# Performance work log

Measured on AMD Instinct MI355X. Metric: run time of the kernel, lower is better.

## Reference

```python
import jax, jax.numpy as jnp
import numpy as np

ITEM_NUM = 50000
TARGET_ITEM_NUM = 50000
EMB = 128
N_LAYERS = 3
N_EDGES = 800000
N_NODES = ITEM_NUM + 1  # forward uses item_emb[:item_num+1]


def gcn_conv(x, row, col, W, b, n):
    """PyG GCNConv: symmetric-normalized aggregation with self-loops.
    out = D^{-1/2} (A + I) D^{-1/2} (x @ W) + b
    """
    h = x @ W  # [n, d]
    loops = jnp.arange(n)
    r = jnp.concatenate([row, loops])  # source
    c = jnp.concatenate([col, loops])  # target
    deg = jax.ops.segment_sum(jnp.ones(r.shape[0], x.dtype), c, num_segments=n)
    dinv = jnp.where(deg > 0, deg ** -0.5, jnp.zeros_like(deg))
    norm = dinv[r] * dinv[c]  # [E+n]
    out = jax.ops.segment_sum(h[r] * norm[:, None], c, num_segments=n)
    return out + b


def setup_inputs() -> dict:
    key = jax.random.key(0)
    k0, k1, k2 = jax.random.split(key, 3)
    edge_index = jax.random.randint(k0, (2, N_EDGES), 0, N_NODES)
    total = ITEM_NUM + TARGET_ITEM_NUM + 1
    # xavier_uniform for embedding table and per-layer GCN weights
    lim_e = float(np.sqrt(6.0 / (total + EMB)))
    item_emb = jax.random.uniform(k1, (total, EMB), jnp.float32, -lim_e, lim_e)
    lim_w = float(np.sqrt(6.0 / (EMB + EMB)))
    W = jax.random.uniform(k2, (N_LAYERS, EMB, EMB), jnp.float32, -lim_w, lim_w)
    b = jnp.zeros((N_LAYERS, EMB), jnp.float32)
    return {"edge_index": edge_index, "item_emb": item_emb, "W": W, "b": b}


def reference(edge_index, item_emb, W, b):
    n = N_NODES
    row, col = edge_index[0], edge_index[1]
    embeds = [item_emb[:n]]
    for i in range(N_LAYERS):
        embeds.append(gcn_conv(embeds[-1], row, col, W[i], b[i], n))
    return sum(embeds)  # [n, EMB], sum over layer embeddings
```

## Files before the change

### kernel.cpp

```cpp
#include <hip/hip_runtime.h>
#include <hip/hip_bf16.h>


constexpr int NN   = 50001;
constexpr int D    = 128;
constexpr int NPAD = 50048;
constexpr int NBK  = 196;
constexpr int CAP  = 7680;
constexpr int ZROW = NPAD - 1;

using bf16x8 = __attribute__((ext_vector_type(8))) short;
using f32x4  = __attribute__((ext_vector_type(4))) float;
using u16x8  = __attribute__((ext_vector_type(8))) unsigned short;
using u32x4  = __attribute__((ext_vector_type(4))) unsigned;

__device__ __forceinline__ ushort f2b(float f) {
    unsigned u = __float_as_uint(f);
    return (ushort)((u + 0x7FFFu + ((u >> 16) & 1u)) >> 16);
}
__device__ __forceinline__ float b2f(ushort u) {
    return __uint_as_float((unsigned)u << 16);
}

__global__ __launch_bounds__(256)
void k_build(const int* __restrict__ row, const int* __restrict__ col,
             int* __restrict__ partCur, unsigned* __restrict__ part,
             const float* __restrict__ W, ushort* __restrict__ Wt,
             const float* __restrict__ emb, ushort* __restrict__ xb, int E, int n) {
    int b = blockIdx.x, t = threadIdx.x;
    if (b < NBK) {
        __shared__ int hist[256];
        __shared__ int base[256];
        hist[t] = 0;
        __syncthreads();
        int e0 = b * 4096;
        unsigned rec[16];
        int bkt[16];
#pragma unroll
        for (int k = 0; k < 16; k++) {
            int e = e0 + k * 256 + t;
            if (e < E) {
                int r = row[e], c = col[e];
                rec[k] = (unsigned)r | ((unsigned)(c & 255) << 16);
                bkt[k] = c >> 8;
                atomicAdd(&hist[bkt[k]], 1);
            } else bkt[k] = -1;
        }
        __syncthreads();
        if (hist[t] > 0) base[t] = t * CAP + atomicAdd(&partCur[t], hist[t]);
        __syncthreads();
#pragma unroll
        for (int k = 0; k < 16; k++) {
            if (bkt[k] >= 0) {
                int pos = atomicAdd(&base[bkt[k]], 1);
                if (pos < (bkt[k] + 1) * CAP) part[pos] = rec[k];
            }
        }
    } else if (b < NBK + 192) {
        int idx = (b - NBK) * 256 + t;
        int l = idx >> 14, rem = idx & 16383;
        int c = rem >> 7, k = rem & 127;
        Wt[idx] = f2b(W[l * D * D + k * D + c]);
    } else {
        int i4 = (b - NBK - 192) * 256 + t;
        if (i4 >= NPAD * (D / 4)) return;
        int r = i4 >> 5;
        if (r < n) {
            float4 v = ((const float4*)emb)[i4];
            ushort4 o; o.x = f2b(v.x); o.y = f2b(v.y); o.z = f2b(v.z); o.w = f2b(v.w);
            ((ushort4*)xb)[i4] = o;
        } else {
            ((ushort4*)xb)[i4] = make_ushort4(0, 0, 0, 0);
        }
    }
}

__global__ __launch_bounds__(256)
void k_scat(const unsigned* __restrict__ part, const int* __restrict__ partCur,
            float* __restrict__ dinv, unsigned* __restrict__ rp,
            ushort* __restrict__ meta, int n) {
    __shared__ int hist[256];
    __shared__ int sm[256];
    __shared__ int off[256];
    __shared__ int cur[256];
    int b = blockIdx.x, t = threadIdx.x;
    int node0 = b * 256;
    int nn = min(256, n - node0);
    int T = min(partCur[b], CAP);
    const unsigned* pb = part + (size_t)b * CAP;
    hist[t] = 0;
    __syncthreads();
    for (int i = t; i < T; i += 256) atomicAdd(&hist[pb[i] >> 16], 1);
    __syncthreads();
    int v = hist[t];
    int pv = (v + 15) & ~15;
    sm[t] = pv;
    __syncthreads();
    for (int ofs = 1; ofs < 256; ofs <<= 1) {
        int u = (t >= ofs) ? sm[t - ofs] : 0;
        __syncthreads();
        sm[t] += u;
        __syncthreads();
    }
    off[t] = sm[t] - pv;
    cur[t] = 0;
    if (t < nn) {
        dinv[node0 + t] = rsqrtf((float)v + 1.0f);
        rp[node0 + t] = (unsigned)(b * CAP + off[t]) | ((unsigned)v << 21);
    }
    __syncthreads();
    for (int i = t; i < T; i += 256) {
        unsigned rec = pb[i];
        int dl = (int)(rec >> 16);
        int pos = off[dl] + atomicAdd(&cur[dl], 1);
        if (pos < CAP) meta[(size_t)b * CAP + pos] = (ushort)(rec & 0xFFFFu);
    }
    int base = off[t];
    for (int p = v; p < pv; p++)
        if (base + p < CAP) meta[(size_t)b * CAP + base + p] = (ushort)ZROW;
}

constexpr int WT_LD = 136;
__global__ __launch_bounds__(256)
void k_gemm_mfma(const ushort* __restrict__ xb, const ushort* __restrict__ WtL,
                 const float* __restrict__ dinv, ushort* __restrict__ h, int n) {
    __shared__ ushort wlds[D * WT_LD];
    for (int idx = threadIdx.x; idx < D * (D / 8); idx += 256) {
        int r = idx >> 4, c8 = (idx & 15) * 8;
        *(uint4*)&wlds[r * WT_LD + c8] = *(const uint4*)&WtL[r * D + c8];
    }
    __syncthreads();

    int wave = threadIdx.x >> 6, lane = threadIdx.x & 63;
    int q = lane >> 4, i = lane & 15;
    int waveRow = blockIdx.x * 128 + wave * 32;

    bf16x8 a[2][4];
#pragma unroll
    for (int rt = 0; rt < 2; rt++) {
        const ushort* base = &xb[(size_t)(waveRow + rt * 16 + i) * D + q * 8];
#pragma unroll
        for (int ks = 0; ks < 4; ks++)
            a[rt][ks] = *(const bf16x8*)(base + ks * 32);
    }

    f32x4 acc[2][8] = {};
#pragma unroll
    for (int ct = 0; ct < 8; ct++) {
        const ushort* wbase = &wlds[(ct * 16 + i) * WT_LD + q * 8];
#pragma unroll
        for (int ks = 0; ks < 4; ks++) {
            bf16x8 bfr = *(const bf16x8*)(wbase + ks * 32);
            acc[0][ct] = __builtin_amdgcn_mfma_f32_16x16x32_bf16(a[0][ks], bfr, acc[0][ct], 0, 0, 0);
            acc[1][ct] = __builtin_amdgcn_mfma_f32_16x16x32_bf16(a[1][ks], bfr, acc[1][ct], 0, 0, 0);
        }
    }

#pragma unroll
    for (int rt = 0; rt < 2; rt++)
#pragma unroll
        for (int r4 = 0; r4 < 4; r4++) {
            int row = waveRow + rt * 16 + q * 4 + r4;
            float dv = (row < n) ? dinv[row] : 0.f;
#pragma unroll
            for (int ct = 0; ct < 8; ct++)
                h[(size_t)row * D + ct * 16 + i] = f2b(acc[rt][ct][r4] * dv);
        }
}

__global__ __launch_bounds__(256)
void k_fused(const unsigned* __restrict__ rp, const ushort* __restrict__ meta,
             const ushort* __restrict__ h_in,
             const float* __restrict__ dinv, const float* __restrict__ bias,
             const ushort* __restrict__ Wn,
             ushort* __restrict__ xb_out, ushort* __restrict__ h_out, int n) {
    __shared__ ushort xlds[16 * WT_LD];
    __shared__ float  sdinv[16];
    int tid  = threadIdx.x;
    int nl   = tid >> 4;
    int l    = tid & 15;
    int node0 = blockIdx.x * 16;
    int node  = node0 + nl;

    u16x8 w = {0, 0, 0, 0, 0, 0, 0, 0};
    float di = 0.f;
    if (node < n) {
        unsigned pk = rp[node];
        int s   = (int)(pk & 0x1FFFFFu);
        int deg = (int)(pk >> 21);
        const ushort* hl = h_in + (l << 3);

        u32x4 sv = *(const u32x4*)(hl + (size_t)node * D);
        di = dinv[node];
        const float4* bp = (const float4*)(bias + (l << 3));
        float4 b0 = bp[0], b1 = bp[1];

        float accL[4], accH[4];
#pragma unroll
        for (int k = 0; k < 4; k++) {
            accL[k] = __uint_as_float(sv[k] << 16);
            accH[k] = __uint_as_float(sv[k] & 0xFFFF0000u);
        }
        for (int j = 0; j < deg; j += 16) {
            u16x8 m0 = *(const u16x8*)&meta[s + j];
            u16x8 m1 = *(const u16x8*)&meta[s + j + 8];
            u32x4 v[16];
#pragma unroll
            for (int u = 0; u < 8; u++) v[u]     = *(const u32x4*)(hl + (size_t)m0[u] * D);
#pragma unroll
            for (int u = 0; u < 8; u++) v[8 + u] = *(const u32x4*)(hl + (size_t)m1[u] * D);
#pragma unroll
            for (int u = 0; u < 16; u++)
#pragma unroll
                for (int k = 0; k < 4; k++) {
                    accL[k] += __uint_as_float(v[u][k] << 16);
                    accH[k] += __uint_as_float(v[u][k] & 0xFFFF0000u);
                }
        }
        w[0] = f2b(fmaf(accL[0], di, b0.x));
        w[1] = f2b(fmaf(accH[0], di, b0.y));
        w[2] = f2b(fmaf(accL[1], di, b0.z));
        w[3] = f2b(fmaf(accH[1], di, b0.w));
        w[4] = f2b(fmaf(accL[2], di, b1.x));
        w[5] = f2b(fmaf(accH[2], di, b1.y));
        w[6] = f2b(fmaf(accL[3], di, b1.z));
        w[7] = f2b(fmaf(accH[3], di, b1.w));
        *(u16x8*)(xb_out + (size_t)node * D + (l << 3)) = w;
    }
    *(u16x8*)&xlds[nl * WT_LD + l * 8] = w;
    if (l == 0) sdinv[nl] = di;
    __syncthreads();

    int wave = tid >> 6, lane = tid & 63;
    int q = lane >> 4, i = lane & 15;

    bf16x8 a[4];
#pragma unroll
    for (int ks = 0; ks < 4; ks++)
        a[ks] = *(const bf16x8*)&xlds[i * WT_LD + ks * 32 + q * 8];

    f32x4 acc[2] = {};
#pragma unroll
    for (int ct = 0; ct < 2; ct++) {
        const ushort* wbase = &Wn[(size_t)(wave * 32 + ct * 16 + i) * D + q * 8];
#pragma unroll
        for (int ks = 0; ks < 4; ks++) {
            bf16x8 bfr = *(const bf16x8*)(wbase + ks * 32);
            acc[ct] = __builtin_amdgcn_mfma_f32_16x16x32_bf16(a[ks], bfr, acc[ct], 0, 0, 0);
        }
    }

#pragma unroll
    for (int r4 = 0; r4 < 4; r4++) {
        int rr = q * 4 + r4;
        float dv = sdinv[rr];
#pragma unroll
        for (int ct = 0; ct < 2; ct++)
            h_out[(size_t)(node0 + rr) * D + wave * 32 + ct * 16 + i] =
                f2b(acc[ct][r4] * dv);
    }
}

__global__ __launch_bounds__(256)
void k_pull_final(const unsigned* __restrict__ rp, const ushort* __restrict__ meta,
                  const ushort* __restrict__ h,
                  const float* __restrict__ dinv, const float* __restrict__ bias,
                  const float* __restrict__ emb, const ushort* __restrict__ x1,
                  const ushort* __restrict__ x2, float* __restrict__ out, int n) {
    int node = blockIdx.x * 16 + (threadIdx.x >> 4);
    int l    = threadIdx.x & 15;
    if (node >= n) return;
    unsigned pk = rp[node];
    int s   = (int)(pk & 0x1FFFFFu);
    int deg = (int)(pk >> 21);
    size_t o = (size_t)node * D + (l << 3);
    const ushort* hl = h + (l << 3);

    u32x4 sv = *(const u32x4*)(hl + (size_t)node * D);
    float di = dinv[node];
    const float4* bp = (const float4*)(bias + (l << 3));
    float4 b0 = bp[0], b1 = bp[1];
    const float4* ep = (const float4*)(emb + o);
    float4 e0 = ep[0], e1 = ep[1];
    u16x8 w1 = *(const u16x8*)(x1 + o);
    u16x8 w2 = *(const u16x8*)(x2 + o);

    float accL[4], accH[4];
#pragma unroll
    for (int k = 0; k < 4; k++) {
        accL[k] = __uint_as_float(sv[k] << 16);
        accH[k] = __uint_as_float(sv[k] & 0xFFFF0000u);
    }
    for (int j = 0; j < deg; j += 16) {
        u16x8 m0 = *(const u16x8*)&meta[s + j];
        u16x8 m1 = *(const u16x8*)&meta[s + j + 8];
        u32x4 v[16];
#pragma unroll
        for (int u = 0; u < 8; u++) v[u]     = *(const u32x4*)(hl + (size_t)m0[u] * D);
#pragma unroll
        for (int u = 0; u < 8; u++) v[8 + u] = *(const u32x4*)(hl + (size_t)m1[u] * D);
#pragma unroll
        for (int u = 0; u < 16; u++)
#pragma unroll
            for (int k = 0; k < 4; k++) {
                accL[k] += __uint_as_float(v[u][k] << 16);
                accH[k] += __uint_as_float(v[u][k] & 0xFFFF0000u);
            }
    }
    f32x4 o0, o1;
    o0[0] = e0.x + b2f(w1[0]) + b2f(w2[0]) + fmaf(accL[0], di, b0.x);
    o0[1] = e0.y + b2f(w1[1]) + b2f(w2[1]) + fmaf(accH[0], di, b0.y);
    o0[2] = e0.z + b2f(w1[2]) + b2f(w2[2]) + fmaf(accL[1], di, b0.z);
    o0[3] = e0.w + b2f(w1[3]) + b2f(w2[3]) + fmaf(accH[1], di, b0.w);
    o1[0] = e1.x + b2f(w1[4]) + b2f(w2[4]) + fmaf(accL[2], di, b1.x);
    o1[1] = e1.y + b2f(w1[5]) + b2f(w2[5]) + fmaf(accH[2], di, b1.y);
    o1[2] = e1.z + b2f(w1[6]) + b2f(w2[6]) + fmaf(accL[3], di, b1.z);
    o1[3] = e1.w + b2f(w1[7]) + b2f(w2[7]) + fmaf(accH[3], di, b1.w);
    __builtin_nontemporal_store(o0, (f32x4*)(out + o));
    __builtin_nontemporal_store(o1, (f32x4*)(out + o) + 1);
}

extern "C" void kernel_launch(void* const* d_in, const int* in_sizes, int n_in,
                              void* d_out, int out_size, void* d_ws, size_t ws_size,
                              hipStream_t stream) {
    const int*   edge = (const int*)d_in[0];
    const float* emb  = (const float*)d_in[1];
    const float* W    = (const float*)d_in[2];
    const float* b    = (const float*)d_in[3];
    float* out = (float*)d_out;

    const int E = in_sizes[0] / 2;
    const int n = NN;
    const int* row = edge;
    const int* col = edge + E;

    char* ws = (char*)d_ws;
    size_t off = 0;
    auto carve = [&](size_t bytes) { char* p = ws + off; off = (off + bytes + 511) / 512 * 512; return p; };
    int*      partCur = (int*)     carve(256 * 4);
    unsigned* part    = (unsigned*)carve((size_t)NBK * CAP * 4);
    ushort*   meta    = (ushort*)  carve((size_t)NBK * CAP * 2);
    unsigned* rp      = (unsigned*)carve((size_t)n * 4);
    float*    dinv    = (float*)   carve((size_t)n * 4);
    ushort*   Wt      = (ushort*)  carve((size_t)3 * D * D * 2);
    ushort*   xb0     = (ushort*)  carve((size_t)NPAD * D * 2);
    ushort*   xb1     = (ushort*)  carve((size_t)NPAD * D * 2);
    ushort*   xb2     = (ushort*)  carve((size_t)NPAD * D * 2);
    ushort*   hA      = (ushort*)  carve((size_t)NPAD * D * 2);
    ushort*   hB      = (ushort*)  carve((size_t)NPAD * D * 2);

    (void)hipMemsetAsync(partCur, 0, 256 * 4, stream);

    const int init_blocks  = (NPAD * (D / 4) + 255) / 256;
    const int build_blocks = NBK + 192 + init_blocks;
    k_build<<<build_blocks, 256, 0, stream>>>(row, col, partCur, part, W, Wt, emb, xb0, E, n);
    k_scat <<<NBK, 256, 0, stream>>>(part, partCur, dinv, rp, meta, n);

    const int gemm_blocks  = NPAD / 128;
    const int fused_blocks = NPAD / 16;
    const int final_blocks = (n + 15) / 16;

    k_gemm_mfma<<<gemm_blocks, 256, 0, stream>>>(xb0, Wt, dinv, hA, n);
    k_fused<<<fused_blocks, 256, 0, stream>>>(rp, meta, hA, dinv, b,
                                              Wt + (size_t)1 * D * D, xb1, hB, n);
    k_fused<<<fused_blocks, 256, 0, stream>>>(rp, meta, hB, dinv, b + D,
                                              Wt + (size_t)2 * D * D, xb2, hA, n);
    k_pull_final<<<final_blocks, 256, 0, stream>>>(rp, meta, hA, dinv, b + 2 * D,
                                                   emb, xb1, xb2, out, n);
}
```

Measured before the change: 240.5 us.

## Fold embedding bf16 conversion into first GEMM and split edge bucketing finer

```diff
diff --git a/kernel.cpp b/kernel.cpp
--- a/kernel.cpp
+++ b/kernel.cpp
@@ -6,7 +6,10 @@
 constexpr int D    = 128;
 constexpr int NPAD = 50048;
 constexpr int NBK  = 196;
-constexpr int CAP  = 7680;
+constexpr int PB   = 784;
+constexpr int PCAP = 7680;
+constexpr int NQB  = NBK * 4;
+constexpr int CAPQ = 2048;
 constexpr int ZROW = NPAD - 1;
 
 using bf16x8 = __attribute__((ext_vector_type(8))) short;
@@ -25,19 +28,18 @@
 __global__ __launch_bounds__(256)
 void k_build(const int* __restrict__ row, const int* __restrict__ col,
              int* __restrict__ partCur, unsigned* __restrict__ part,
-             const float* __restrict__ W, ushort* __restrict__ Wt,
-             const float* __restrict__ emb, ushort* __restrict__ xb, int E, int n) {
+             const float* __restrict__ W, ushort* __restrict__ Wt, int E) {
     int b = blockIdx.x, t = threadIdx.x;
-    if (b < NBK) {
+    if (b < PB) {
         __shared__ int hist[256];
         __shared__ int base[256];
         hist[t] = 0;
         __syncthreads();
-        int e0 = b * 4096;
-        unsigned rec[16];
-        int bkt[16];
-#pragma unroll
-        for (int k = 0; k < 16; k++) {
+        int e0 = b * 1024;
+        unsigned rec[4];
+        int bkt[4];
+#pragma unroll
+        for (int k = 0; k < 4; k++) {
             int e = e0 + k * 256 + t;
             if (e < E) {
                 int r = row[e], c = col[e];
@@ -47,31 +49,20 @@
             } else bkt[k] = -1;
         }
         __syncthreads();
-        if (hist[t] > 0) base[t] = t * CAP + atomicAdd(&partCur[t], hist[t]);
-        __syncthreads();
-#pragma unroll
-        for (int k = 0; k < 16; k++) {
+        if (hist[t] > 0) base[t] = t * PCAP + atomicAdd(&partCur[t], hist[t]);
+        __syncthreads();
+#pragma unroll
+        for (int k = 0; k < 4; k++) {
             if (bkt[k] >= 0) {
                 int pos = atomicAdd(&base[bkt[k]], 1);
-                if (pos < (bkt[k] + 1) * CAP) part[pos] = rec[k];
+                if (pos < (bkt[k] + 1) * PCAP) part[pos] = rec[k];
             }
         }
-    } else if (b < NBK + 192) {
-        int idx = (b - NBK) * 256 + t;
+    } else {
+        int idx = (b - PB) * 256 + t;
         int l = idx >> 14, rem = idx & 16383;
         int c = rem >> 7, k = rem & 127;
         Wt[idx] = f2b(W[l * D * D + k * D + c]);
-    } else {
-        int i4 = (b - NBK - 192) * 256 + t;
-        if (i4 >= NPAD * (D / 4)) return;
-        int r = i4 >> 5;
-        if (r < n) {
-            float4 v = ((const float4*)emb)[i4];
-            ushort4 o; o.x = f2b(v.x); o.y = f2b(v.y); o.z = f2b(v.z); o.w = f2b(v.w);
-            ((ushort4*)xb)[i4] = o;
-        } else {
-            ((ushort4*)xb)[i4] = make_ushort4(0, 0, 0, 0);
-        }
     }
 }
 
@@ -79,51 +70,63 @@
 void k_scat(const unsigned* __restrict__ part, const int* __restrict__ partCur,
             float* __restrict__ dinv, unsigned* __restrict__ rp,
             ushort* __restrict__ meta, int n) {
-    __shared__ int hist[256];
-    __shared__ int sm[256];
-    __shared__ int off[256];
-    __shared__ int cur[256];
+    __shared__ int hist[64];
+    __shared__ int sm[64];
+    __shared__ int off[64];
+    __shared__ int cur[64];
     int b = blockIdx.x, t = threadIdx.x;
-    int node0 = b * 256;
-    int nn = min(256, n - node0);
-    int T = min(partCur[b], CAP);
-    const unsigned* pb = part + (size_t)b * CAP;
-    hist[t] = 0;
-    __syncthreads();
-    for (int i = t; i < T; i += 256) atomicAdd(&hist[pb[i] >> 16], 1);
-    __syncthreads();
-    int v = hist[t];
-    int pv = (v + 15) & ~15;
-    sm[t] = pv;
-    __syncthreads();
-    for (int ofs = 1; ofs < 256; ofs <<= 1) {
-        int u = (t >= ofs) ? sm[t - ofs] : 0;
-        __syncthreads();
-        sm[t] += u;
-        __syncthreads();
-    }
-    off[t] = sm[t] - pv;
-    cur[t] = 0;
-    if (t < nn) {
-        dinv[node0 + t] = rsqrtf((float)v + 1.0f);
-        rp[node0 + t] = (unsigned)(b * CAP + off[t]) | ((unsigned)v << 21);
+    int B = b >> 2, q = b & 3;
+    int node0 = B * 256 + q * 64;
+    int T = min(partCur[B], PCAP);
+    const unsigned* pb = part + (size_t)B * PCAP;
+    if (t < 64) hist[t] = 0;
+    __syncthreads();
+    for (int i = t; i < T; i += 256) {
+        int dl = (int)(pb[i] >> 16);
+        if ((dl >> 6) == q) atomicAdd(&hist[dl & 63], 1);
+    }
+    __syncthreads();
+    if (t < 64) sm[t] = (hist[t] + 15) & ~15;
+    __syncthreads();
+    for (int ofs = 1; ofs < 64; ofs <<= 1) {
+        int u = 0;
+        if (t >= ofs && t < 64) u = sm[t - ofs];
+        __syncthreads();
+        if (t < 64) sm[t] += u;
+        __syncthreads();
+    }
+    if (t < 64) {
+        int v = hist[t];
+        off[t] = sm[t] - ((v + 15) & ~15);
+        cur[t] = 0;
+        int node = node0 + t;
+        if (node < n) {
+            dinv[node] = rsqrtf((float)v + 1.0f);
+            rp[node] = (unsigned)(b * CAPQ + off[t]) | ((unsigned)v << 21);
+        }
     }
     __syncthreads();
     for (int i = t; i < T; i += 256) {
         unsigned rec = pb[i];
         int dl = (int)(rec >> 16);
-        int pos = off[dl] + atomicAdd(&cur[dl], 1);
-        if (pos < CAP) meta[(size_t)b * CAP + pos] = (ushort)(rec & 0xFFFFu);
-    }
-    int base = off[t];
-    for (int p = v; p < pv; p++)
-        if (base + p < CAP) meta[(size_t)b * CAP + base + p] = (ushort)ZROW;
+        if ((dl >> 6) == q) {
+            int m = dl & 63;
+            int pos = off[m] + atomicAdd(&cur[m], 1);
+            if (pos < CAPQ) meta[(size_t)b * CAPQ + pos] = (ushort)(rec & 0xFFFFu);
+        }
+    }
+    if (t < 64) {
+        int v = hist[t], pv = (v + 15) & ~15;
+        int base = off[t];
+        for (int p = v; p < pv; p++)
+            if (base + p < CAPQ) meta[(size_t)b * CAPQ + base + p] = (ushort)ZROW;
+    }
 }
 
 constexpr int WT_LD = 136;
 __global__ __launch_bounds__(256)
-void k_gemm_mfma(const ushort* __restrict__ xb, const ushort* __restrict__ WtL,
-                 const float* __restrict__ dinv, ushort* __restrict__ h, int n) {
+void k_gemm0(const float* __restrict__ emb, const ushort* __restrict__ WtL,
+             const float* __restrict__ dinv, ushort* __restrict__ h, int n) {
     __shared__ ushort wlds[D * WT_LD];
     for (int idx = threadIdx.x; idx < D * (D / 8); idx += 256) {
         int r = idx >> 4, c8 = (idx & 15) * 8;
@@ -138,10 +141,18 @@
     bf16x8 a[2][4];
 #pragma unroll
     for (int rt = 0; rt < 2; rt++) {
-        const ushort* base = &xb[(size_t)(waveRow + rt * 16 + i) * D + q * 8];
-#pragma unroll
-        for (int ks = 0; ks < 4; ks++)
-            a[rt][ks] = *(const bf16x8*)(base + ks * 32);
+        const float* base = emb + (size_t)(waveRow + rt * 16 + i) * D + q * 8;
+#pragma unroll
+        for (int ks = 0; ks < 4; ks++) {
+            float4 v0 = *(const float4*)(base + ks * 32);
+            float4 v1 = *(const float4*)(base + ks * 32 + 4);
+            bf16x8 aa;
+            aa[0] = (short)f2b(v0.x); aa[1] = (short)f2b(v0.y);
+            aa[2] = (short)f2b(v0.z); aa[3] = (short)f2b(v0.w);
+            aa[4] = (short)f2b(v1.x); aa[5] = (short)f2b(v1.y);
+            aa[6] = (short)f2b(v1.z); aa[7] = (short)f2b(v1.w);
+            a[rt][ks] = aa;
+        }
     }
 
     f32x4 acc[2][8] = {};
@@ -338,12 +349,11 @@
     size_t off = 0;
     auto carve = [&](size_t bytes) { char* p = ws + off; off = (off + bytes + 511) / 512 * 512; return p; };
     int*      partCur = (int*)     carve(256 * 4);
-    unsigned* part    = (unsigned*)carve((size_t)NBK * CAP * 4);
-    ushort*   meta    = (ushort*)  carve((size_t)NBK * CAP * 2);
+    unsigned* part    = (unsigned*)carve((size_t)NBK * PCAP * 4);
+    ushort*   meta    = (ushort*)  carve((size_t)NQB * CAPQ * 2);
     unsigned* rp      = (unsigned*)carve((size_t)n * 4);
     float*    dinv    = (float*)   carve((size_t)n * 4);
     ushort*   Wt      = (ushort*)  carve((size_t)3 * D * D * 2);
-    ushort*   xb0     = (ushort*)  carve((size_t)NPAD * D * 2);
     ushort*   xb1     = (ushort*)  carve((size_t)NPAD * D * 2);
     ushort*   xb2     = (ushort*)  carve((size_t)NPAD * D * 2);
     ushort*   hA      = (ushort*)  carve((size_t)NPAD * D * 2);
@@ -351,16 +361,15 @@
 
     (void)hipMemsetAsync(partCur, 0, 256 * 4, stream);
 
-    const int init_blocks  = (NPAD * (D / 4) + 255) / 256;
-    const int build_blocks = NBK + 192 + init_blocks;
-    k_build<<<build_blocks, 256, 0, stream>>>(row, col, partCur, part, W, Wt, emb, xb0, E, n);
-    k_scat <<<NBK, 256, 0, stream>>>(part, partCur, dinv, rp, meta, n);
+    const int build_blocks = PB + 192;
+    k_build<<<build_blocks, 256, 0, stream>>>(row, col, partCur, part, W, Wt, E);
+    k_scat <<<NQB, 256, 0, stream>>>(part, partCur, dinv, rp, meta, n);
 
     const int gemm_blocks  = NPAD / 128;
     const int fused_blocks = NPAD / 16;
     const int final_blocks = (n + 15) / 16;
 
-    k_gemm_mfma<<<gemm_blocks, 256, 0, stream>>>(xb0, Wt, dinv, hA, n);
+    k_gemm0<<<gemm_blocks, 256, 0, stream>>>(emb, Wt, dinv, hA, n);
     k_fused<<<fused_blocks, 256, 0, stream>>>(rp, meta, hA, dinv, b,
                                               Wt + (size_t)1 * D * D, xb1, hB, n);
     k_fused<<<fused_blocks, 256, 0, stream>>>(rp, meta, hB, dinv, b + D,
```

After: 250.7 us. 4.2% more time.
